# Performance work log

Hardware: AMD Instinct MI355X
Metric: run time of the kernel (lower is better)

## Reference

```python
import jax, jax.numpy as jnp
import numpy as np

N_NODES = 100000
N_EDGES = 1600000
F_IN = 256
HID = 16
HEADS = 8
N_CLASSES = 16
NEG_SLOPE = 0.2  # DGL GATConv default leaky_relu slope


def setup_inputs() -> dict:
    key = jax.random.key(0)
    ks = jax.random.split(key, 12)
    feat = jax.random.normal(ks[0], (N_NODES, F_IN), dtype=jnp.float32)
    src = jax.random.randint(ks[1], (N_EDGES,), 0, N_NODES, dtype=jnp.int32)
    dst = jax.random.randint(ks[2], (N_EDGES,), 0, N_NODES, dtype=jnp.int32)
    s1 = 1.0 / np.sqrt(F_IN)
    s2 = 1.0 / np.sqrt(HID * HEADS)
    W1 = jax.random.normal(ks[3], (F_IN, HEADS * HID), dtype=jnp.float32) * s1
    al1 = jax.random.normal(ks[4], (HEADS, HID), dtype=jnp.float32) * s1
    ar1 = jax.random.normal(ks[5], (HEADS, HID), dtype=jnp.float32) * s1
    b1 = jnp.zeros((HEADS * HID,), dtype=jnp.float32)
    W2 = jax.random.normal(ks[6], (HEADS * HID, N_CLASSES), dtype=jnp.float32) * s2
    al2 = jax.random.normal(ks[7], (1, N_CLASSES), dtype=jnp.float32) * s2
    ar2 = jax.random.normal(ks[8], (1, N_CLASSES), dtype=jnp.float32) * s2
    b2 = jnp.zeros((N_CLASSES,), dtype=jnp.float32)
    return {"feat": feat, "src": src, "dst": dst,
            "W1": W1, "al1": al1, "ar1": ar1, "b1": b1,
            "W2": W2, "al2": al2, "ar2": ar2, "b2": b2}


def gat_conv(x, src, dst, W, attn_l, attn_r, bias, n_heads, out_dim):
    # x: [N, F_in]; W: [F_in, H*D]; attn_l/attn_r: [H, D]; bias: [H*D]
    n = x.shape[0]
    h = (x @ W).reshape(n, n_heads, out_dim)              # [N,H,D]
    el = jnp.einsum('nhd,hd->nh', h, attn_l)              # [N,H]
    er = jnp.einsum('nhd,hd->nh', h, attn_r)              # [N,H]
    e = jax.nn.leaky_relu(el[src] + er[dst], NEG_SLOPE)   # [E,H]
    # segment softmax over incoming edges of each destination node
    e_max = jax.ops.segment_max(e, dst, num_segments=n)   # [N,H] (-inf for isolated)
    ex = jnp.exp(e - e_max[dst])                          # [E,H]
    denom = jax.ops.segment_sum(ex, dst, num_segments=n)  # [N,H]
    a = ex / denom[dst]                                   # [E,H]
    msg = a[:, :, None] * h[src]                          # [E,H,D]
    out = jax.ops.segment_sum(msg, dst, num_segments=n)   # [N,H,D]
    return out + bias.reshape(1, n_heads, out_dim)


def reference(feat, src, dst, W1, al1, ar1, b1, W2, al2, ar2, b2):
    h = gat_conv(feat, src, dst, W1, al1, ar1, b1, HEADS, HID)   # [N,H,HID]
    h = jax.nn.elu(h.reshape(h.shape[0], -1))                     # [N,H*HID]
    h = gat_conv(h, src, dst, W2, al2, ar2, b2, 1, N_CLASSES)     # [N,1,C]
    h = h.reshape(h.shape[0], -1)
    return jax.nn.log_softmax(h, axis=1)
```

## Files before the change

kernel.cpp:

```cpp
#include <hip/hip_runtime.h>

#define N_NODES 100000
#define N_EDGES 1600000
#define F_IN 256
#define HD1 128
#define HEADS 8
#define HID 16
#define NC 16
#define NEG_SLOPE 0.2f
#define LOG2E 1.44269504f

#define BKT_NODES 512
#define NBKT ((N_NODES + BKT_NODES - 1) / BKT_NODES)
#define P1_EPB 8192
#define P1_BLOCKS ((N_EDGES + P1_EPB - 1) / P1_EPB)

__device__ __forceinline__ float leaky(float x){ return x > 0.f ? x : NEG_SLOPE * x; }
__device__ __forceinline__ unsigned short f2bf(float f){
    unsigned u = __float_as_uint(f);
    u += 0x7fff + ((u >> 16) & 1);
    return (unsigned short)(u >> 16);
}
__device__ __forceinline__ float bf2f(unsigned short s){
    return __uint_as_float((unsigned)s << 16);
}
__device__ __forceinline__ unsigned char f2fp8(float v){
    return (unsigned char)(__builtin_amdgcn_cvt_pk_fp8_f32(v, v, 0, false) & 0xff);
}
__device__ __forceinline__ unsigned cvtpk_bf16(float lo, float hi){
    unsigned r;
    asm("v_cvt_pk_bf16_f32 %0, %1, %2" : "=v"(r) : "v"(lo), "v"(hi));
    return r;
}

typedef __bf16 bf16x8 __attribute__((ext_vector_type(8)));
typedef short short8 __attribute__((ext_vector_type(8)));
typedef float f32x4 __attribute__((ext_vector_type(4)));
typedef float f32x2 __attribute__((ext_vector_type(2)));


__global__ void __launch_bounds__(256) k_p1hist(const int* __restrict__ dst, int* __restrict__ bucketTotal){
    __shared__ int h[NBKT];
    int t = threadIdx.x;
    for (int i = t; i < NBKT; i += 256) h[i] = 0;
    __syncthreads();
    int base = blockIdx.x * P1_EPB;
    int m = min(P1_EPB, N_EDGES - base);
    for (int i = t; i < m; i += 256) atomicAdd(&h[(unsigned)dst[base + i] >> 9], 1);
    __syncthreads();
    for (int i = t; i < NBKT; i += 256) if (h[i]) atomicAdd(&bucketTotal[i], h[i]);
}

__global__ void __launch_bounds__(256) k_p1scan(const int* __restrict__ bucketTotal,
                                                int* __restrict__ bucketBase, int* __restrict__ bucketCursor,
                                                int* __restrict__ off){
    __shared__ int sc[256];
    int t = threadIdx.x;
    int v = (t < NBKT) ? bucketTotal[t] : 0;
    sc[t] = v; __syncthreads();
    for (int o = 1; o < 256; o <<= 1){
        int a = (t >= o) ? sc[t - o] : 0;
        __syncthreads();
        sc[t] += a;
        __syncthreads();
    }
    if (t < NBKT){
        int b = sc[t] - v;
        bucketBase[t] = b;
        bucketCursor[t] = b;
    }
    if (t == 0){ bucketBase[NBKT] = N_EDGES; off[N_NODES] = N_EDGES; }
}

__global__ void __launch_bounds__(256) k_p1bin(const int* __restrict__ src, const int* __restrict__ dst,
                                               int* __restrict__ bucketCursor,
                                               unsigned long long* __restrict__ pairs){
    __shared__ unsigned long long pl[P1_EPB];
    __shared__ int h[NBKT];
    __shared__ int dl[NBKT];
    __shared__ int sc[256];
    int t = threadIdx.x;
    for (int i = t; i < NBKT; i += 256) h[i] = 0;
    __syncthreads();
    int base = blockIdx.x * P1_EPB;
    int m = min(P1_EPB, N_EDGES - base);
    for (int i = t; i < m; i += 256) atomicAdd(&h[(unsigned)dst[base + i] >> 9], 1);
    __syncthreads();
    int v = (t < NBKT) ? h[t] : 0;
    sc[t] = v; __syncthreads();
    for (int o = 1; o < 256; o <<= 1){
        int a = (t >= o) ? sc[t - o] : 0;
        __syncthreads();
        sc[t] += a;
        __syncthreads();
    }
    if (t < NBKT){
        int ex = sc[t] - v;
        int gb = v ? atomicAdd(&bucketCursor[t], v) : 0;
        dl[t] = gb - ex;
        h[t] = ex;
    }
    __syncthreads();
    for (int i = t; i < m; i += 256){
        int d = dst[base + i], s = src[base + i];
        int b = (unsigned)d >> 9;
        int p = atomicAdd(&h[b], 1);
        pl[p] = ((unsigned long long)(unsigned)d << 32) | (unsigned)s;
    }
    __syncthreads();
    for (int i = t; i < m; i += 256){
        unsigned long long pr = pl[i];
        int b = (unsigned)(pr >> 32) >> 9;
        pairs[i + dl[b]] = pr;
    }
}

__global__ void __launch_bounds__(256) k_p2place(const unsigned long long* __restrict__ pairs,
                                                 const int* __restrict__ bucketBase,
                                                 int* __restrict__ off, int* __restrict__ csr_src){
    __shared__ int degc[BKT_NODES];
    __shared__ int sc2[BKT_NODES];
    int t = threadIdx.x;
    int b = blockIdx.x;
    int node0 = b * BKT_NODES;
    int nmax = min(BKT_NODES, N_NODES - node0);
    int p0 = bucketBase[b], p1 = bucketBase[b + 1];
    int m = p1 - p0;
    for (int i = t; i < BKT_NODES; i += 256) degc[i] = 0;
    __syncthreads();
    for (int i = t; i < m; i += 256){
        int d = (int)(pairs[p0 + i] >> 32) - node0;
        atomicAdd(&degc[d], 1);
    }
    __syncthreads();
    for (int i = t; i < BKT_NODES; i += 256) sc2[i] = degc[i];
    __syncthreads();
    for (int o = 1; o < BKT_NODES; o <<= 1){
        int i0 = t, i1 = t + 256;
        int a0 = (i0 >= o) ? sc2[i0 - o] : 0;
        int a1 = (i1 >= o) ? sc2[i1 - o] : 0;
        __syncthreads();
        sc2[i0] += a0; sc2[i1] += a1;
        __syncthreads();
    }
    for (int i = t; i < BKT_NODES; i += 256){
        int cur = p0 + sc2[i] - degc[i];
        if (i < nmax) off[node0 + i] = cur;
        degc[i] = cur;
    }
    __syncthreads();
    for (int i = t; i < m; i += 256){
        unsigned long long pr = pairs[p0 + i];
        int d = (int)(pr >> 32) - node0;
        int pos = atomicAdd(&degc[d], 1);
        csr_src[pos] = (int)(unsigned)pr;
    }
}


__global__ void __launch_bounds__(256) k_splitW(const float* __restrict__ W1,
                                                short* __restrict__ WTH){
    int i = blockIdx.x * 256 + threadIdx.x;
    if (i >= F_IN * HD1) return;
    int k = i >> 7, n = i & 127;
    int idx = n * 256 + (k ^ ((n & 7) << 3));
    WTH[idx] = (short)f2bf(W1[i]);
}


__device__ __forceinline__ short8 pack8(float4 f0, float4 f1){
    uint4 p;
    p.x = cvtpk_bf16(f0.x, f0.y);
    p.y = cvtpk_bf16(f0.z, f0.w);
    p.z = cvtpk_bf16(f1.x, f1.y);
    p.w = cvtpk_bf16(f1.z, f1.w);
    return __builtin_bit_cast(short8, p);
}

__global__ void __launch_bounds__(512, 4) k_gemm1m(const float* __restrict__ feat,
                                                   const short* __restrict__ WTH,
                                                   unsigned char* __restrict__ h1f8){
    __shared__ short sWH[F_IN * HD1];
    int t = threadIdx.x;
    {
        const short8* gh = (const short8*)WTH;
        short8* sh = (short8*)sWH;
        for (int i = t; i < 4096; i += 512) sh[i] = gh[i];
    }
    __syncthreads();

    int wid = t >> 6, lane = t & 63;
    int m16 = lane & 15, kg = lane >> 4;
    int rowb = blockIdx.x * 256 + wid * 32;

    f32x4 acc[2][8];
    #pragma unroll
    for (int a = 0; a < 2; a++)
        #pragma unroll
        for (int b = 0; b < 8; b++)
            acc[a][b] = (f32x4){0.f, 0.f, 0.f, 0.f};

    int r0 = rowb + m16;       if (r0 > N_NODES - 1) r0 = N_NODES - 1;
    int r1 = rowb + 16 + m16;  if (r1 > N_NODES - 1) r1 = N_NODES - 1;
    const float* fp0 = feat + (size_t)r0 * F_IN;
    const float* fp1 = feat + (size_t)r1 * F_IN;

    #pragma unroll
    for (int ks = 0; ks < 8; ks++){
        int kbase = ks * 32 + kg * 8;
        short8 a0, a1;
        {
            const float4* p = (const float4*)(fp0 + kbase);
            a0 = pack8(p[0], p[1]);
        }
        {
            const float4* p = (const float4*)(fp1 + kbase);
            a1 = pack8(p[0], p[1]);
        }
        bf16x8 AH0 = __builtin_bit_cast(bf16x8, a0);
        bf16x8 AH1 = __builtin_bit_cast(bf16x8, a1);
        #pragma unroll
        for (int c = 0; c < 8; c++){
            int n = (c << 4) + m16;
            int kk = kbase ^ ((n & 7) << 3);
            bf16x8 bh = __builtin_bit_cast(bf16x8, *(const short8*)(sWH + n * 256 + kk));
            acc[0][c] = __builtin_amdgcn_mfma_f32_16x16x32_bf16(AH0, bh, acc[0][c], 0, 0, 0);
            acc[1][c] = __builtin_amdgcn_mfma_f32_16x16x32_bf16(AH1, bh, acc[1][c], 0, 0, 0);
        }
    }

    #pragma unroll
    for (int rf = 0; rf < 2; rf++){
        #pragma unroll
        for (int c = 0; c < 8; c++){
            #pragma unroll
            for (int r = 0; r < 4; r++){
                int row = rowb + rf * 16 + kg * 4 + r;
                if (row < N_NODES){
                    int col = c * 16 + m16;
                    h1f8[(size_t)row * HD1 + col] = f2fp8(acc[rf][c][r]);
                }
            }
        }
    }
}


__global__ void __launch_bounds__(256) k_attn1(const unsigned char* __restrict__ h1f8,
                                               const float* __restrict__ al1, const float* __restrict__ ar1,
                                               unsigned short* __restrict__ el1b, float* __restrict__ er1){
    int i = blockIdx.x * 256 + threadIdx.x;
    if (i >= N_NODES * HEADS) return;
    int n = i >> 3, h = i & 7;
    const unsigned* hp = (const unsigned*)(h1f8 + (size_t)n * HD1 + h * HID);
    float pe = 0.f, pr = 0.f;
    #pragma unroll
    for (int j = 0; j < 4; j++){
        unsigned u = hp[j];
        float x0 = __builtin_amdgcn_cvt_f32_fp8(u, 0);
        float x1 = __builtin_amdgcn_cvt_f32_fp8(u, 1);
        float x2 = __builtin_amdgcn_cvt_f32_fp8(u, 2);
        float x3 = __builtin_amdgcn_cvt_f32_fp8(u, 3);
        const float4 a = ((const float4*)(al1 + h * HID))[j];
        const float4 r = ((const float4*)(ar1 + h * HID))[j];
        pe += x0 * a.x + x1 * a.y + x2 * a.z + x3 * a.w;
        pr += x0 * r.x + x1 * r.y + x2 * r.z + x3 * r.w;
    }
    el1b[i] = f2bf(pe * LOG2E);
    er1[i] = pr * LOG2E;
}


__global__ void __launch_bounds__(256) k_agg1(const int* __restrict__ off, const int* __restrict__ csr_src,
                                              const unsigned short* __restrict__ el1b,
                                              const float* __restrict__ er1,
                                              const unsigned char* __restrict__ h1f8,
                                              const float* __restrict__ b1,
                                              unsigned short* __restrict__ x2b){
    int wid = threadIdx.x >> 6, lane = threadIdx.x & 63;
    int n = blockIdx.x * 4 + wid;
    if (n >= N_NODES) return;
    int jb = off[n], je = off[n + 1];
    int sub = lane >> 4;
    int q = lane & 15;
    int hh = q >> 1;
    float ern = er1[n * HEADS + hh];
    float a0=0.f,a1=0.f,a2=0.f,a3=0.f,a4=0.f,a5=0.f,a6=0.f,a7=0.f,wsum=0.f;

    #pragma unroll 4
    for (int j = jb; j < je; j += 4){
        int jj = j + sub;
        int jc = (jj < je) ? jj : je - 1;
        int s = csr_src[jc];
        float el = bf2f(el1b[s * HEADS + hh]);
        float wv = (jj < je) ? __builtin_amdgcn_exp2f(leaky(el + ern)) : 0.f;
        wsum += wv;
        uint2 u = *(const uint2*)(h1f8 + (((size_t)s) << 7) + (q << 3));
        f32x2 p0 = __builtin_amdgcn_cvt_pk_f32_fp8(u.x, 0);
        f32x2 p1 = __builtin_amdgcn_cvt_pk_f32_fp8(u.x, 1);
        f32x2 p2 = __builtin_amdgcn_cvt_pk_f32_fp8(u.y, 0);
        f32x2 p3 = __builtin_amdgcn_cvt_pk_f32_fp8(u.y, 1);
        a0 += wv * p0.x; a1 += wv * p0.y;
        a2 += wv * p1.x; a3 += wv * p1.y;
        a4 += wv * p2.x; a5 += wv * p2.y;
        a6 += wv * p3.x; a7 += wv * p3.y;
    }

    a0 += __shfl_xor(a0, 16); a0 += __shfl_xor(a0, 32);
    a1 += __shfl_xor(a1, 16); a1 += __shfl_xor(a1, 32);
    a2 += __shfl_xor(a2, 16); a2 += __shfl_xor(a2, 32);
    a3 += __shfl_xor(a3, 16); a3 += __shfl_xor(a3, 32);
    a4 += __shfl_xor(a4, 16); a4 += __shfl_xor(a4, 32);
    a5 += __shfl_xor(a5, 16); a5 += __shfl_xor(a5, 32);
    a6 += __shfl_xor(a6, 16); a6 += __shfl_xor(a6, 32);
    a7 += __shfl_xor(a7, 16); a7 += __shfl_xor(a7, 32);
    wsum += __shfl_xor(wsum, 16); wsum += __shfl_xor(wsum, 32);

    if (sub == 0){
        float inv = (je > jb) ? 1.f / wsum : 0.f;
        float o0 = a0*inv, o1 = a1*inv, o2 = a2*inv, o3 = a3*inv;
        float o4 = a4*inv, o5 = a5*inv, o6 = a6*inv, o7 = a7*inv;
        float4 bv0 = *(const float4*)(b1 + (q << 3));
        float4 bv1 = *(const float4*)(b1 + (q << 3) + 4);
        o0 += bv0.x; o1 += bv0.y; o2 += bv0.z; o3 += bv0.w;
        o4 += bv1.x; o5 += bv1.y; o6 += bv1.z; o7 += bv1.w;
        o0 = o0 > 0.f ? o0 : __expf(o0) - 1.f;
        o1 = o1 > 0.f ? o1 : __expf(o1) - 1.f;
        o2 = o2 > 0.f ? o2 : __expf(o2) - 1.f;
        o3 = o3 > 0.f ? o3 : __expf(o3) - 1.f;
        o4 = o4 > 0.f ? o4 : __expf(o4) - 1.f;
        o5 = o5 > 0.f ? o5 : __expf(o5) - 1.f;
        o6 = o6 > 0.f ? o6 : __expf(o6) - 1.f;
        o7 = o7 > 0.f ? o7 : __expf(o7) - 1.f;
        uint4 ov;
        ov.x = cvtpk_bf16(o0, o1);
        ov.y = cvtpk_bf16(o2, o3);
        ov.z = cvtpk_bf16(o4, o5);
        ov.w = cvtpk_bf16(o6, o7);
        *(uint4*)(x2b + (size_t)n * HD1 + (q << 3)) = ov;
    }
}


__global__ void __launch_bounds__(256) k_gemm2(const unsigned short* __restrict__ x2b, const float* __restrict__ W2,
                                               const float* __restrict__ al2, const float* __restrict__ ar2,
                                               unsigned short* __restrict__ h2e, float* __restrict__ er2){
    __shared__ float sW[HD1 * NC];
    __shared__ float sX[16 * HD1];
    int t = threadIdx.x;
    for (int i = t; i < (HD1 * NC) / 4; i += 256)
        ((float4*)sW)[i] = ((const float4*)W2)[i];
    int r = t >> 4, c = t & 15;
    float a2 = al2[c], r2 = ar2[c];
    for (int g = blockIdx.x; g * 16 < N_NODES; g += gridDim.x){
        int rowb = g * 16;
        __syncthreads();
        {
            ushort4 v = ((const ushort4*)(x2b + (size_t)rowb * HD1))[t * 2];
            ushort4 v2 = ((const ushort4*)(x2b + (size_t)rowb * HD1))[t * 2 + 1];
            float4 f0 = { bf2f(v.x), bf2f(v.y), bf2f(v.z), bf2f(v.w) };
            float4 f1 = { bf2f(v2.x), bf2f(v2.y), bf2f(v2.z), bf2f(v2.w) };
            ((float4*)sX)[t * 2] = f0;
            ((float4*)sX)[t * 2 + 1] = f1;
        }
        __syncthreads();
        float acc = 0.f;
        #pragma unroll 8
        for (int k = 0; k < HD1; k++)
            acc += sX[r * HD1 + k] * sW[k * NC + c];
        int row = rowb + r;
        h2e[(size_t)row * 32 + c] = f2bf(acc);
        float pe = acc * a2, pr = acc * r2;
        #pragma unroll
        for (int d = 1; d < 16; d <<= 1){ pe += __shfl_xor(pe, d); pr += __shfl_xor(pr, d); }
        if (c == 0){
            *(float*)(h2e + (size_t)row * 32 + 16) = pe * LOG2E;
            er2[row] = pr * LOG2E;
        }
    }
}


__global__ void __launch_bounds__(256) k_agg2(const int* __restrict__ off, const int* __restrict__ csr_src,
                                              const float* __restrict__ er2,
                                              const unsigned short* __restrict__ h2e, const float* __restrict__ b2,
                                              float* __restrict__ out){
    int t = threadIdx.x;
    int sub = t >> 4;
    int c = t & 15;
    int n = blockIdx.x * 16 + sub;
    if (n >= N_NODES) return;
    int jb = off[n], je = off[n + 1];
    float er = er2[n];
    float accA = 0.f, accB = 0.f, wsA = 0.f, wsB = 0.f;
    int j = jb;
    for (; j + 1 < je; j += 2){
        int s0 = csr_src[j];
        int s1 = csr_src[j + 1];
        const unsigned short* r0 = h2e + (size_t)s0 * 32;
        const unsigned short* r1 = h2e + (size_t)s1 * 32;
        float el0 = *(const float*)(r0 + 16);
        float el1 = *(const float*)(r1 + 16);
        float w0 = __builtin_amdgcn_exp2f(leaky(el0 + er));
        float w1 = __builtin_amdgcn_exp2f(leaky(el1 + er));
        float v0 = bf2f(r0[c]);
        float v1 = bf2f(r1[c]);
        wsA += w0; accA += w0 * v0;
        wsB += w1; accB += w1 * v1;
    }
    if (j < je){
        int s0 = csr_src[j];
        const unsigned short* r0 = h2e + (size_t)s0 * 32;
        float el0 = *(const float*)(r0 + 16);
        float w0 = __builtin_amdgcn_exp2f(leaky(el0 + er));
        wsA += w0; accA += w0 * bf2f(r0[c]);
    }
    float acc = accA + accB, wsum = wsA + wsB;
    float o = (je > jb) ? acc / wsum : 0.f;
    o += b2[c];
    float m = o;
    #pragma unroll
    for (int d = 1; d < 16; d <<= 1) m = fmaxf(m, __shfl_xor(m, d));
    float ex = __expf(o - m);
    #pragma unroll
    for (int d = 1; d < 16; d <<= 1) ex += __shfl_xor(ex, d);
    out[(size_t)n * NC + c] = o - m - __logf(ex);
}


extern "C" void kernel_launch(void* const* d_in, const int* in_sizes, int n_in,
                              void* d_out, int out_size, void* d_ws, size_t ws_size,
                              hipStream_t stream){
    const float* feat = (const float*)d_in[0];
    const int*   src  = (const int*)d_in[1];
    const int*   dst  = (const int*)d_in[2];
    const float* W1   = (const float*)d_in[3];
    const float* al1  = (const float*)d_in[4];
    const float* ar1  = (const float*)d_in[5];
    const float* b1   = (const float*)d_in[6];
    const float* W2   = (const float*)d_in[7];
    const float* al2  = (const float*)d_in[8];
    const float* ar2  = (const float*)d_in[9];
    const float* b2   = (const float*)d_in[10];
    float* out = (float*)d_out;

    char* w = (char*)d_ws;
    auto alloc = [&](size_t bytes) -> char* {
        char* p = w;
        w += (bytes + 255) & ~(size_t)255;
        return p;
    };
    int*   off      = (int*)alloc((size_t)(N_NODES + 1) * 4);
    int*   csr_src  = (int*)alloc((size_t)N_EDGES * 4);
    unsigned long long* pairs = (unsigned long long*)alloc((size_t)N_EDGES * 8);
    int*   bucketTotal  = (int*)alloc((size_t)(NBKT + 1) * 4);
    int*   bucketBase   = (int*)alloc((size_t)(NBKT + 1) * 4);
    int*   bucketCursor = (int*)alloc((size_t)(NBKT + 1) * 4);
    unsigned char*  h1f8 = (unsigned char*)alloc((size_t)N_NODES * HD1);
    unsigned short* el1b = (unsigned short*)alloc((size_t)N_NODES * HEADS * 2);
    float* er1v    = (float*)alloc((size_t)N_NODES * HEADS * 4);
    unsigned short* x2b = (unsigned short*)alloc((size_t)N_NODES * HD1 * 2);
    unsigned short* h2e = (unsigned short*)alloc((size_t)N_NODES * 64);
    float* er2v    = (float*)alloc((size_t)N_NODES * 4);
    short* WTH     = (short*)alloc((size_t)F_IN * HD1 * 2);

    hipMemsetAsync(bucketTotal, 0, (size_t)(NBKT + 1) * 4, stream);
    k_p1hist<<<P1_BLOCKS, 256, 0, stream>>>(dst, bucketTotal);
    k_p1scan<<<1, 256, 0, stream>>>(bucketTotal, bucketBase, bucketCursor, off);
    k_p1bin<<<P1_BLOCKS, 256, 0, stream>>>(src, dst, bucketCursor, pairs);
    k_p2place<<<NBKT, 256, 0, stream>>>(pairs, bucketBase, off, csr_src);

    k_splitW<<<(F_IN * HD1 + 255) / 256, 256, 0, stream>>>(W1, WTH);
    k_gemm1m<<<(N_NODES + 255) / 256, 512, 0, stream>>>(feat, WTH, h1f8);
    k_attn1<<<(N_NODES * HEADS + 255) / 256, 256, 0, stream>>>(h1f8, al1, ar1, el1b, er1v);

    k_agg1<<<(N_NODES + 3) / 4, 256, 0, stream>>>(off, csr_src, el1b, er1v, h1f8, b1, x2b);

    k_gemm2<<<1024, 256, 0, stream>>>(x2b, W2, al2, ar2, h2e, er2v);
    k_agg2<<<(N_NODES + 15) / 16, 256, 0, stream>>>(off, csr_src, er2v, h2e, b2, out);
}
```

Before: 222.8 us.

## Store per-block histograms, fold splitW into hist kernel, tweak gemm/attn/agg2

The histogram kernel now writes per-block bucket counts to global memory instead of atomically summing them. The scan reduces those counts and the bin kernel reuses its own block's counts rather than recomputing the histogram, which drops the memset and a second pass over dst. The W1 bf16 split is merged into the histogram launch as extra blocks, removing one kernel launch. It also adds s_setprio around the MFMA loop in gemm1, switches attn1 to a single uint4 load, and adds an unroll pragma in agg2. The single-block scan now serially sums 196 partial rows per bucket, which adds latency to that step.

```diff
diff --git a/kernel.cpp b/kernel.cpp
--- a/kernel.cpp
+++ b/kernel.cpp
@@ -14,6 +14,7 @@
 #define NBKT ((N_NODES + BKT_NODES - 1) / BKT_NODES)
 #define P1_EPB 8192
 #define P1_BLOCKS ((N_EDGES + P1_EPB - 1) / P1_EPB)
+#define SPLITW_BLOCKS ((F_IN * HD1) / 256)
 
 __device__ __forceinline__ float leaky(float x){ return x > 0.f ? x : NEG_SLOPE * x; }
 __device__ __forceinline__ unsigned short f2bf(float f){
@@ -39,24 +40,35 @@
 typedef float f32x2 __attribute__((ext_vector_type(2)));
 
 
-__global__ void __launch_bounds__(256) k_p1hist(const int* __restrict__ dst, int* __restrict__ bucketTotal){
+__global__ void __launch_bounds__(256) k_p1hist(const int* __restrict__ dst, int* __restrict__ bucketPart,
+                                                const float* __restrict__ W1, short* __restrict__ WTH){
+    int t = threadIdx.x;
+    int bid = blockIdx.x;
+    if (bid >= P1_BLOCKS){
+        int i = (bid - P1_BLOCKS) * 256 + t;
+        int k = i >> 7, n = i & 127;
+        int idx = n * 256 + (k ^ ((n & 7) << 3));
+        WTH[idx] = (short)f2bf(W1[i]);
+        return;
+    }
     __shared__ int h[NBKT];
-    int t = threadIdx.x;
     for (int i = t; i < NBKT; i += 256) h[i] = 0;
     __syncthreads();
-    int base = blockIdx.x * P1_EPB;
+    int base = bid * P1_EPB;
     int m = min(P1_EPB, N_EDGES - base);
     for (int i = t; i < m; i += 256) atomicAdd(&h[(unsigned)dst[base + i] >> 9], 1);
     __syncthreads();
-    for (int i = t; i < NBKT; i += 256) if (h[i]) atomicAdd(&bucketTotal[i], h[i]);
-}
-
-__global__ void __launch_bounds__(256) k_p1scan(const int* __restrict__ bucketTotal,
+    for (int i = t; i < NBKT; i += 256) bucketPart[bid * NBKT + i] = h[i];
+}
+
+__global__ void __launch_bounds__(256) k_p1scan(const int* __restrict__ bucketPart,
                                                 int* __restrict__ bucketBase, int* __restrict__ bucketCursor,
                                                 int* __restrict__ off){
     __shared__ int sc[256];
     int t = threadIdx.x;
-    int v = (t < NBKT) ? bucketTotal[t] : 0;
+    int v = 0;
+    if (t < NBKT)
+        for (int b = 0; b < P1_BLOCKS; b++) v += bucketPart[b * NBKT + t];
     sc[t] = v; __syncthreads();
     for (int o = 1; o < 256; o <<= 1){
         int a = (t >= o) ? sc[t - o] : 0;
@@ -73,6 +85,7 @@
 }
 
 __global__ void __launch_bounds__(256) k_p1bin(const int* __restrict__ src, const int* __restrict__ dst,
+                                               const int* __restrict__ bucketPart,
                                                int* __restrict__ bucketCursor,
                                                unsigned long long* __restrict__ pairs){
     __shared__ unsigned long long pl[P1_EPB];
@@ -80,13 +93,8 @@
     __shared__ int dl[NBKT];
     __shared__ int sc[256];
     int t = threadIdx.x;
-    for (int i = t; i < NBKT; i += 256) h[i] = 0;
-    __syncthreads();
-    int base = blockIdx.x * P1_EPB;
-    int m = min(P1_EPB, N_EDGES - base);
-    for (int i = t; i < m; i += 256) atomicAdd(&h[(unsigned)dst[base + i] >> 9], 1);
-    __syncthreads();
-    int v = (t < NBKT) ? h[t] : 0;
+    int bid = blockIdx.x;
+    int v = (t < NBKT) ? bucketPart[bid * NBKT + t] : 0;
     sc[t] = v; __syncthreads();
     for (int o = 1; o < 256; o <<= 1){
         int a = (t >= o) ? sc[t - o] : 0;
@@ -101,6 +109,8 @@
         h[t] = ex;
     }
     __syncthreads();
+    int base = bid * P1_EPB;
+    int m = min(P1_EPB, N_EDGES - base);
     for (int i = t; i < m; i += 256){
         int d = dst[base + i], s = src[base + i];
         int b = (unsigned)d >> 9;
@@ -155,16 +165,6 @@
         int pos = atomicAdd(&degc[d], 1);
         csr_src[pos] = (int)(unsigned)pr;
     }
-}
-
-
-__global__ void __launch_bounds__(256) k_splitW(const float* __restrict__ W1,
-                                                short* __restrict__ WTH){
-    int i = blockIdx.x * 256 + threadIdx.x;
-    if (i >= F_IN * HD1) return;
-    int k = i >> 7, n = i & 127;
-    int idx = n * 256 + (k ^ ((n & 7) << 3));
-    WTH[idx] = (short)f2bf(W1[i]);
 }
 
 
@@ -219,6 +219,7 @@
         }
         bf16x8 AH0 = __builtin_bit_cast(bf16x8, a0);
         bf16x8 AH1 = __builtin_bit_cast(bf16x8, a1);
+        __builtin_amdgcn_s_setprio(1);
         #pragma unroll
         for (int c = 0; c < 8; c++){
             int n = (c << 4) + m16;
@@ -227,6 +228,7 @@
             acc[0][c] = __builtin_amdgcn_mfma_f32_16x16x32_bf16(AH0, bh, acc[0][c], 0, 0, 0);
             acc[1][c] = __builtin_amdgcn_mfma_f32_16x16x32_bf16(AH1, bh, acc[1][c], 0, 0, 0);
         }
+        __builtin_amdgcn_s_setprio(0);
     }
 
     #pragma unroll
@@ -252,11 +254,12 @@
     int i = blockIdx.x * 256 + threadIdx.x;
     if (i >= N_NODES * HEADS) return;
     int n = i >> 3, h = i & 7;
-    const unsigned* hp = (const unsigned*)(h1f8 + (size_t)n * HD1 + h * HID);
+    uint4 hv = *(const uint4*)(h1f8 + (size_t)n * HD1 + h * HID);
+    unsigned uu[4] = {hv.x, hv.y, hv.z, hv.w};
     float pe = 0.f, pr = 0.f;
     #pragma unroll
     for (int j = 0; j < 4; j++){
-        unsigned u = hp[j];
+        unsigned u = uu[j];
         float x0 = __builtin_amdgcn_cvt_f32_fp8(u, 0);
         float x1 = __builtin_amdgcn_cvt_f32_fp8(u, 1);
         float x2 = __builtin_amdgcn_cvt_f32_fp8(u, 2);
@@ -394,6 +397,7 @@
     float er = er2[n];
     float accA = 0.f, accB = 0.f, wsA = 0.f, wsB = 0.f;
     int j = jb;
+    #pragma unroll 2
     for (; j + 1 < je; j += 2){
         int s0 = csr_src[j];
         int s1 = csr_src[j + 1];
@@ -453,7 +457,7 @@
     int*   off      = (int*)alloc((size_t)(N_NODES + 1) * 4);
     int*   csr_src  = (int*)alloc((size_t)N_EDGES * 4);
     unsigned long long* pairs = (unsigned long long*)alloc((size_t)N_EDGES * 8);
-    int*   bucketTotal  = (int*)alloc((size_t)(NBKT + 1) * 4);
+    int*   bucketPart   = (int*)alloc((size_t)P1_BLOCKS * NBKT * 4);
     int*   bucketBase   = (int*)alloc((size_t)(NBKT + 1) * 4);
     int*   bucketCursor = (int*)alloc((size_t)(NBKT + 1) * 4);
     unsigned char*  h1f8 = (unsigned char*)alloc((size_t)N_NODES * HD1);
@@ -464,13 +468,11 @@
     float* er2v    = (float*)alloc((size_t)N_NODES * 4);
     short* WTH     = (short*)alloc((size_t)F_IN * HD1 * 2);
 
-    hipMemsetAsync(bucketTotal, 0, (size_t)(NBKT + 1) * 4, stream);
-    k_p1hist<<<P1_BLOCKS, 256, 0, stream>>>(dst, bucketTotal);
-    k_p1scan<<<1, 256, 0, stream>>>(bucketTotal, bucketBase, bucketCursor, off);
-    k_p1bin<<<P1_BLOCKS, 256, 0, stream>>>(src, dst, bucketCursor, pairs);
+    k_p1hist<<<P1_BLOCKS + SPLITW_BLOCKS, 256, 0, stream>>>(dst, bucketPart, W1, WTH);
+    k_p1scan<<<1, 256, 0, stream>>>(bucketPart, bucketBase, bucketCursor, off);
+    k_p1bin<<<P1_BLOCKS, 256, 0, stream>>>(src, dst, bucketPart, bucketCursor, pairs);
     k_p2place<<<NBKT, 256, 0, stream>>>(pairs, bucketBase, off, csr_src);
 
-    k_splitW<<<(F_IN * HD1 + 255) / 256, 256, 0, stream>>>(W1, WTH);
     k_gemm1m<<<(N_NODES + 255) / 256, 512, 0, stream>>>(feat, WTH, h1f8);
     k_attn1<<<(N_NODES * HEADS + 255) / 256, 256, 0, stream>>>(h1f8, al1, ar1, el1b, er1v);
 
```

After: 204.5 us. -8.2%, faster.
